# Performance work log

Measured on AMD Instinct MI355X. Metric: run time of the kernel, lower is better.

Reference implementation:

```python
import jax, jax.numpy as jnp
import numpy as np

N = 10                       # qubits
DIM = 2 ** N                 # statevector dim
B = 2048                     # batch
T = 8                        # timesteps
INV_SQRT = float(1.0 / np.sqrt(DIM))
H_GATE = jnp.asarray((1.0 / np.sqrt(2.0)) * np.array([[1, 1], [1, -1]], dtype=np.complex64))
T_GATE = jnp.asarray(np.array([[1, 0], [0, np.exp(1j * np.pi / 4)]], dtype=np.complex64))
# random CZ pairs in the candidate circuit are drawn once at circuit-build time (np.random > 0.7)
_rng = np.random.RandomState(0)
CAND_CZ = [(i, j) for i in range(N) for j in range(i + 1, N) if _rng.random() > 0.7]


def _ry(t):
    c, s = jnp.cos(t / 2), jnp.sin(t / 2)
    return jnp.stack([jnp.stack([c, -s], -1), jnp.stack([s, c], -1)], -2).astype(jnp.complex64)


def _rz(t):
    e = jnp.exp(-0.5j * t.astype(jnp.complex64))
    z = jnp.zeros_like(e)
    return jnp.stack([jnp.stack([e, z], -1), jnp.stack([z, jnp.conj(e)], -1)], -2)


def _rx(t):
    c = jnp.cos(t / 2).astype(jnp.complex64)
    s = (-1j * jnp.sin(t / 2).astype(jnp.complex64))
    return jnp.stack([jnp.stack([c, s], -1), jnp.stack([s, c], -1)], -2)


def _app1(st, q, U):
    # apply a 1-qubit gate on qubit q; U is [2,2] or batched [B,2,2]
    b = st.shape[0]
    s = st.reshape(b, 2 ** q, 2, DIM // 2 ** (q + 1))
    if U.ndim == 2:
        s = jnp.einsum('ij,bljr->blir', U, s)
    else:
        s = jnp.einsum('bij,bljr->blir', U, s)
    return s.reshape(b, DIM)


def _cz(st, q1, q2):  # q1 < q2
    b = st.shape[0]
    s = st.reshape(b, 2 ** q1, 2, 2 ** (q2 - q1 - 1), 2, DIM // 2 ** (q2 + 1))
    s = s.at[:, :, 1, :, 1, :].multiply(-1.0)
    return s.reshape(b, DIM)


def _cnot(st, qc, qt):  # qc < qt
    b = st.shape[0]
    s = st.reshape(b, 2 ** qc, 2, 2 ** (qt - qc - 1), 2, DIM // 2 ** (qt + 1))
    c0 = s[:, :, 0]                      # [b, A, M, 2, C]
    c1 = jnp.flip(s[:, :, 1], axis=3)    # flip target bit when control == 1
    return jnp.stack([c0, c1], axis=2).reshape(b, DIM)


def _uniform(b):
    # initialize_quantum_state: H on every qubit from |0...0> = uniform real state
    return jnp.full((b, DIM), INV_SQRT, dtype=jnp.complex64)


def _measure(st):
    # <Z>, <X>, <Y> per qubit (get_measurement_operators) -> [b, 3N]
    b = st.shape[0]
    feats = []
    for q in range(N):
        s = st.reshape(b, 2 ** q, 2, DIM // 2 ** (q + 1))
        a0, a1 = s[:, :, 0, :], s[:, :, 1, :]
        p0 = jnp.sum(jnp.abs(a0) ** 2, axis=(1, 2))
        p1 = jnp.sum(jnp.abs(a1) ** 2, axis=(1, 2))
        cr = jnp.sum(jnp.conj(a0) * a1, axis=(1, 2))
        feats += [p0 - p1, 2 * jnp.real(cr), 2 * jnp.imag(cr)]
    return jnp.stack(feats, -1)


def circ_forget(p):  # p [b, N]
    s = _uniform(p.shape[0])
    for q in range(N):
        s = _app1(s, q, _ry(p[:, q]))
    for q in range(0, N - 1, 2):
        s = _cz(s, q, q + 1)
    for q in range(N):
        s = _app1(s, q, T_GATE)
    return _measure(s)


def circ_input(p):  # p [b, 2N]
    s = _uniform(p.shape[0])
    for q in range(N):
        s = _app1(s, q, _ry(p[:, 2 * q]))
        s = _app1(s, q, _rz(p[:, 2 * q + 1]))
    for q in range(N - 1):
        s = _cnot(s, q, q + 1)
    return _measure(s)


def circ_output(p):  # p [b, N]
    s = _uniform(p.shape[0])
    for q in range(N):
        s = _app1(s, q, _rx(p[:, q]))
    for q in range(N - 1):
        s = _cnot(s, q, q + 1)
    return _measure(s)


def circ_candidate(p):  # p [b, 3N]
    s = _uniform(p.shape[0])
    for q in range(N):  # second H layer of the candidate gate
        s = _app1(s, q, H_GATE)
    for q in range(N):
        s = _app1(s, q, _rz(p[:, 3 * q]))
        s = _app1(s, q, _ry(p[:, 3 * q + 1]))
        s = _app1(s, q, _rz(p[:, 3 * q + 2]))
    for (i, j) in CAND_CZ:
        s = _cz(s, i, j)
    return _measure(s)


def circ_memory(p):  # p [b, N]
    s = _uniform(p.shape[0])
    for q in range(N):
        s = _app1(s, q, _ry(p[:, q]))
    for q in range(0, N - 1, 2):
        s = _cz(s, q, q + 1)
    return _measure(s)


def circ_temporal(t):  # t [b]
    s = _uniform(t.shape[0])
    nm = N // 2
    for i in range(min(nm, N - nm)):           # entangle memory<->hidden
        s = _cnot(s, i, nm + i)
    s = _app1(s, 0, H_GATE)                    # GHZ-style entanglement
    for i in range(1, N):
        s = _cnot(s, 0, i)
    for q in range(N):                         # time evolution
        s = _app1(s, q, _rz(0.1 * t))
        s = _app1(s, q, _rx(0.05 * t))
    for q in range(N - 1):
        s = _cnot(s, q, q + 1)
        s = _app1(s, q + 1, _rz(0.2 * t))
        s = _cnot(s, q, q + 1)
    return _measure(s)


def _forward(x, Wx, Wh, bias, R):
    Bsz = x.shape[0]

    def step(carry, x_t):
        h, c = carry
        p = x_t @ Wx + h @ Wh + bias            # [B, 8N+1] circuit angles
        pf, pi = p[:, :N], p[:, N:3 * N]
        po, pc = p[:, 3 * N:4 * N], p[:, 4 * N:7 * N]
        pm, pt = p[:, 7 * N:8 * N], p[:, 8 * N]
        f = jax.nn.sigmoid(circ_forget(pf) @ R[0])
        i_ = jax.nn.sigmoid(circ_input(pi) @ R[1])
        o = jax.nn.sigmoid(circ_output(po) @ R[2])
        g = jnp.tanh(circ_candidate(pc) @ R[3])
        mq = jax.nn.sigmoid(circ_memory(pm) @ R[4])
        tm = jnp.tanh(circ_temporal(pt) @ R[5])
        c_new = (f * c + i_ * g) * mq           # quantum memory update
        h_new = o * jnp.tanh(c_new) + 0.1 * tm  # temporal evolution contribution
        return (h_new, c_new), h_new

    h0 = jnp.zeros((Bsz, N), jnp.float32)
    c0 = jnp.zeros((Bsz, N), jnp.float32)
    _, hs = jax.lax.scan(step, (h0, c0), jnp.swapaxes(x, 0, 1))
    return jnp.swapaxes(hs, 0, 1)               # [B, T, N]


def setup_inputs() -> dict:
    key = jax.random.key(0)
    k1, k2, k3, k4 = jax.random.split(key, 4)
    x = jax.random.normal(k1, (B, T, N), dtype=jnp.float32)
    Wx = 0.3 * jax.random.normal(k2, (N, 8 * N + 1), dtype=jnp.float32)
    Wh = 0.3 * jax.random.normal(k3, (N, 8 * N + 1), dtype=jnp.float32)
    bias = jnp.zeros((8 * N + 1,), dtype=jnp.float32)
    R = 0.3 * jax.random.normal(k4, (6, 3 * N, N), dtype=jnp.float32)
    return {"x": x, "Wx": Wx, "Wh": Wh, "bias": bias, "R": R}


def reference(x, Wx, Wh, bias, R):
    return _forward(x, Wx, Wh, bias, R)
```

## Files before the change

### kernel.cpp

```cpp
#include <hip/hip_runtime.h>

#define NQ 10
#define NP 81
#define TT 8

__device__ __forceinline__ float sigm(float z) {
    z = fminf(fmaxf(z, -30.f), 30.f);
    return 1.f / (1.f + __expf(-z));
}
__device__ __forceinline__ float tanh_(float z) {
    z = fminf(fmaxf(z, -15.f), 15.f);
    float e = __expf(2.f * z);
    return (e - 1.f) / (e + 1.f);
}

__global__ __launch_bounds__(256) void qlstm_kernel(
    const float* __restrict__ x, const float* __restrict__ Wx,
    const float* __restrict__ Wh, const float* __restrict__ bias,
    const float* __restrict__ R, float* __restrict__ out) {

    __shared__ float x_s[8 * 8 * 12];
    __shared__ float h_s[8 * 12];
    __shared__ float c_s[8 * 10];
    __shared__ float p_s[8 * NP];
    __shared__ float ft_s[30 * 40];
    __shared__ float g_s[8 * 5 * 10];

    const int tid = threadIdx.x;
    const int bbase = blockIdx.x * 8;

    for (int i = tid; i < 640; i += 256) {
        int g = i / 80, r = i - g * 80;
        int t = r / 10, k = r - t * 10;
        x_s[g * 96 + t * 12 + k] = x[(size_t)bbase * 80 + i];
    }
    if (tid < 96) h_s[tid] = 0.f;
    if (tid < 80) c_s[tid] = 0.f;

    const int j1 = tid & 127;
    const int g0 = (tid >> 7) * 4;
    const bool p1act = (j1 < NP);
    float wx[NQ], wh[NQ], bj = 0.f;
    if (p1act) {
#pragma unroll
        for (int k = 0; k < NQ; ++k) { wx[k] = Wx[k * NP + j1]; wh[k] = Wh[k * NP + j1]; }
        bj = bias[j1];
    }

    const int gB1 = tid / 50, remB1 = tid - gB1 * 50;
    const int gt1 = remB1 / 10, k1 = remB1 - gt1 * 10;
    const int gR1 = gt1 + (gt1 >= 2 ? 1 : 0);
    float r1[30];
#pragma unroll
    for (int f = 0; f < 30; ++f) r1[f] = R[gR1 * 300 + f * 10 + k1];
    const bool hasj2 = (tid < 144);
    const int jb2 = tid + 256;
    const int gB2 = jb2 / 50, remB2 = jb2 - gB2 * 50;
    const int gt2 = remB2 / 10, k2 = remB2 - gt2 * 10;
    const int gR2 = gt2 + (gt2 >= 2 ? 1 : 0);
    float r2[30];
    if (hasj2) {
#pragma unroll
        for (int f = 0; f < 30; ++f) r2[f] = R[gR2 * 300 + f * 10 + k2];
    }

    const bool hasC = (tid < 80);
    const int gC = tid / 10, kC = tid - gC * 10;
    float o_val = 0.f;
    if (hasC) {
        float s = 0.f;
#pragma unroll
        for (int q = 0; q < NQ; ++q) s += R[600 + (3 * q + 1) * 10 + kC];
        o_val = sigm(s);
    }

    const int wv = tid >> 6, ln = tid & 63;
    __syncthreads();

    for (int t = 0; t < TT; ++t) {
        if (p1act) {
            float acc[4];
#pragma unroll
            for (int i = 0; i < 4; ++i) acc[i] = bj;
#pragma unroll
            for (int i = 0; i < 4; ++i) {
                const float* xr = &x_s[(g0 + i) * 96 + t * 12];
                const float* hr = &h_s[(g0 + i) * 12];
#pragma unroll
                for (int k = 0; k < NQ; ++k)
                    acc[i] = fmaf(xr[k], wx[k], fmaf(hr[k], wh[k], acc[i]));
            }
#pragma unroll
            for (int i = 0; i < 4; ++i) p_s[(g0 + i) * NP + j1] = acc[i];
        }
        __syncthreads();

        if (wv == 0 && ln < 8) {
            const int g = ln;
            const float* pp = &p_s[g * NP];
            float sa[NQ], ca[NQ], ftl[30];
#pragma unroll
            for (int q = 0; q < NQ; ++q) __sincosf(pp[q], &sa[q], &ca[q]);
            const float r2c = 0.70710678118654752f;
#pragma unroll
            for (int m = 0; m < 5; ++m) {
                int q = 2 * m, q1 = q + 1;
                ftl[3 * q] = -sa[q];
                float v = -r2c * ca[q] * sa[q1];
                ftl[3 * q + 1] = v; ftl[3 * q + 2] = v;
                ftl[3 * q1] = -sa[q1];
                float v2 = -r2c * ca[q1] * sa[q];
                ftl[3 * q1 + 1] = v2; ftl[3 * q1 + 2] = v2;
            }
#pragma unroll
            for (int f = 0; f < 30; ++f) ft_s[f * 40 + g * 5 + 0] = ftl[f];
        } else if (wv == 1 && ln < 8) {
            const int g = ln;
            const float* pp = &p_s[g * NP];
            float sa[NQ], ca[NQ], sb[NQ], cb[NQ], ftl[30];
#pragma unroll
            for (int q = 0; q < NQ; ++q) __sincosf(pp[10 + 2 * q], &sa[q], &ca[q]);
#pragma unroll
            for (int q = 0; q < NQ; ++q) __sincosf(pp[11 + 2 * q], &sb[q], &cb[q]);
            float xx[NQ], uu[NQ];
#pragma unroll
            for (int q = 0; q < NQ; ++q) { xx[q] = ca[q] * cb[q]; uu[q] = ca[q] * sb[q]; }
            float Zprev = 1.f;
#pragma unroll
            for (int q = 0; q < NQ; ++q) {
                float zq = Zprev * (-sa[q]);
                float xn = (q < 9) ? xx[q + 1] : 1.f;
                ftl[3 * q] = zq;
                ftl[3 * q + 1] = xx[q] * xn;
                ftl[3 * q + 2] = uu[q] * Zprev * xn;
                Zprev = zq;
            }
#pragma unroll
            for (int f = 0; f < 30; ++f) ft_s[f * 40 + g * 5 + 1] = ftl[f];
        } else if (wv == 2 && ln < 8) {
            const int g = ln;
            const float* pp = &p_s[g * NP];
            float sb[NQ], cb[NQ], sc[NQ], cc[NQ], ftl[30];
#pragma unroll
            for (int q = 0; q < NQ; ++q) __sincosf(pp[41 + 3 * q], &sb[q], &cb[q]);
#pragma unroll
            for (int q = 0; q < NQ; ++q) __sincosf(pp[42 + 3 * q], &sc[q], &cc[q]);
            float P[NQ];
            P[0] = cb[2] * cb[8] * cb[9];
            P[1] = cb[3] * cb[6];
            P[2] = cb[0] * cb[3] * cb[4] * cb[5] * cb[6] * cb[7] * cb[9];
            P[3] = cb[1] * cb[2] * cb[7];
            P[4] = cb[2] * cb[6];
            P[5] = cb[2] * cb[9];
            P[6] = cb[1] * cb[2] * cb[4];
            P[7] = cb[2] * cb[3];
            P[8] = cb[0];
            P[9] = cb[0] * cb[2] * cb[5];
#pragma unroll
            for (int q = 0; q < NQ; ++q) {
                ftl[3 * q] = cb[q];
                float m = sb[q] * P[q];
                ftl[3 * q + 1] = m * cc[q];
                ftl[3 * q + 2] = m * sc[q];
            }
#pragma unroll
            for (int f = 0; f < 30; ++f) ft_s[f * 40 + g * 5 + 2] = ftl[f];
        } else if (wv == 3 && ln < 16) {
            if (ln < 8) {
                const int g = ln;
                float tt = p_s[g * NP + 80];
                float s2, c2, s4, c4, s6, c6, s8, c8, ftl[30];
                __sincosf(0.050f * tt, &s2, &c2);
                __sincosf(0.100f * tt, &s4, &c4);
                __sincosf(0.150f * tt, &s6, &c6);
                __sincosf(0.200f * tt, &s8, &c8);
                (void)s4;
                float z0 = c2;
                float zs = 0.5f * (c2 - c6);
                float mre = 0.5f * c4;
                float mim = 0.25f * (s2 + s6);
                float E0re = c8, E0im = z0 * s8;
                float Esre = c8, Esim = zs * s8;
                float cr0re = 0.5f * s2 * Esim;
                float cr0im = -0.5f * s2 * Esre;
                float EEre = Esre * Esre - Esim * Esim, EEim = 2.f * Esre * Esim;
                float EOre = E0re * Esre - E0im * Esim, EOim = E0re * Esim + E0im * Esre;
                float cr1re = mre * EOre - mim * EOim, cr1im = mre * EOim + mim * EOre;
                float crmre = mre * EEre - mim * EEim, crmim = mre * EEim + mim * EEre;
                float cr9re = mre * Esre - mim * Esim, cr9im = mre * Esim + mim * Esre;
                ftl[0] = z0; ftl[1] = 2.f * cr0re; ftl[2] = 2.f * cr0im;
                ftl[3] = zs; ftl[4] = 2.f * cr1re; ftl[5] = 2.f * cr1im;
#pragma unroll
                for (int q = 2; q <= 8; ++q) {
                    ftl[3 * q] = zs; ftl[3 * q + 1] = 2.f * crmre; ftl[3 * q + 2] = 2.f * crmim;
                }
                ftl[27] = zs; ftl[28] = 2.f * cr9re; ftl[29] = 2.f * cr9im;
#pragma unroll
                for (int f = 0; f < 30; ++f) ft_s[f * 40 + g * 5 + 4] = ftl[f];
            } else {
                const int g = ln - 8;
                const float* pp = &p_s[g * NP];
                float sa[NQ], ca[NQ], ftl[30];
#pragma unroll
                for (int q = 0; q < NQ; ++q) __sincosf(pp[70 + q], &sa[q], &ca[q]);
#pragma unroll
                for (int m = 0; m < 5; ++m) {
                    int q = 2 * m, q1 = q + 1;
                    ftl[3 * q] = -sa[q];
                    ftl[3 * q + 1] = -ca[q] * sa[q1];
                    ftl[3 * q + 2] = 0.f;
                    ftl[3 * q1] = -sa[q1];
                    ftl[3 * q1 + 1] = -ca[q1] * sa[q];
                    ftl[3 * q1 + 2] = 0.f;
                }
#pragma unroll
                for (int f = 0; f < 30; ++f) ft_s[f * 40 + g * 5 + 3] = ftl[f];
            }
        }
        __syncthreads();

        {
            const int base1 = gB1 * 5 + gt1;
            float acc = 0.f;
#pragma unroll
            for (int f = 0; f < 30; ++f) acc = fmaf(ft_s[f * 40 + base1], r1[f], acc);
            g_s[tid] = acc;
            if (hasj2) {
                const int base2 = gB2 * 5 + gt2;
                float acc2 = 0.f;
#pragma unroll
                for (int f = 0; f < 30; ++f) acc2 = fmaf(ft_s[f * 40 + base2], r2[f], acc2);
                g_s[jb2] = acc2;
            }
        }
        __syncthreads();

        if (hasC) {
            float f = sigm(g_s[gC * 50 + 0 * 10 + kC]);
            float ii = sigm(g_s[gC * 50 + 1 * 10 + kC]);
            float gg = tanh_(g_s[gC * 50 + 2 * 10 + kC]);
            float mq = sigm(g_s[gC * 50 + 3 * 10 + kC]);
            float tm = tanh_(g_s[gC * 50 + 4 * 10 + kC]);
            float cn = (f * c_s[gC * 10 + kC] + ii * gg) * mq;
            float hn = o_val * tanh_(cn) + 0.1f * tm;
            c_s[gC * 10 + kC] = cn;
            h_s[gC * 12 + kC] = hn;
            out[(size_t)(bbase + gC) * 80 + t * 10 + kC] = hn;
        }
        __syncthreads();
    }
}

extern "C" void kernel_launch(void* const* d_in, const int* in_sizes, int n_in,
                              void* d_out, int out_size, void* d_ws, size_t ws_size,
                              hipStream_t stream) {
    const float* x = (const float*)d_in[0];
    const float* Wx = (const float*)d_in[1];
    const float* Wh = (const float*)d_in[2];
    const float* bias = (const float*)d_in[3];
    const float* R = (const float*)d_in[4];
    float* out = (float*)d_out;

    qlstm_kernel<<<dim3(256), dim3(256), 0, stream>>>(x, Wx, Wh, bias, R, out);
}
```

Measured before the change: 80.07 us.

## Map one batch element per wavefront and replace block barriers with wave-local sync

Restructures the recurrent kernel so each 64-lane wavefront owns one batch element, using wave barriers instead of block-wide __syncthreads. Input projections for all timesteps are precomputed before the loop. Per-lane sincos replaces the serial per-thread trig loops, and feature and gate stages are spread across lanes with float4 LDS reads. The grid doubles to 512 blocks for more parallelism. The cost is that more lanes sit idle in some stages, and correctness now depends on wave-synchronous LDS ordering.

```diff
diff --git a/kernel.cpp b/kernel.cpp
--- a/kernel.cpp
+++ b/kernel.cpp
@@ -3,6 +3,15 @@
 #define NQ 10
 #define NP 81
 #define TT 8
+
+#define PXO   0
+#define SOFF  648
+#define COFF  712
+#define FTO   776
+#define GOFF  956
+#define HOFF  1008
+#define XOFF  1020
+#define WWORDS 1100
 
 __device__ __forceinline__ float sigm(float z) {
     z = fminf(fmaxf(z, -30.f), 30.f);
@@ -19,235 +28,191 @@
     const float* __restrict__ Wh, const float* __restrict__ bias,
     const float* __restrict__ R, float* __restrict__ out) {
 
-    __shared__ float x_s[8 * 8 * 12];
-    __shared__ float h_s[8 * 12];
-    __shared__ float c_s[8 * 10];
-    __shared__ float p_s[8 * NP];
-    __shared__ float ft_s[30 * 40];
-    __shared__ float g_s[8 * 5 * 10];
-
+    __shared__ __align__(16) float lds_all[4 * WWORDS];
     const int tid = threadIdx.x;
-    const int bbase = blockIdx.x * 8;
-
-    for (int i = tid; i < 640; i += 256) {
-        int g = i / 80, r = i - g * 80;
-        int t = r / 10, k = r - t * 10;
-        x_s[g * 96 + t * 12 + k] = x[(size_t)bbase * 80 + i];
-    }
-    if (tid < 96) h_s[tid] = 0.f;
-    if (tid < 80) c_s[tid] = 0.f;
-
-    const int j1 = tid & 127;
-    const int g0 = (tid >> 7) * 4;
-    const bool p1act = (j1 < NP);
-    float wx[NQ], wh[NQ], bj = 0.f;
-    if (p1act) {
-#pragma unroll
-        for (int k = 0; k < NQ; ++k) { wx[k] = Wx[k * NP + j1]; wh[k] = Wh[k * NP + j1]; }
-        bj = bias[j1];
-    }
-
-    const int gB1 = tid / 50, remB1 = tid - gB1 * 50;
-    const int gt1 = remB1 / 10, k1 = remB1 - gt1 * 10;
-    const int gR1 = gt1 + (gt1 >= 2 ? 1 : 0);
-    float r1[30];
-#pragma unroll
-    for (int f = 0; f < 30; ++f) r1[f] = R[gR1 * 300 + f * 10 + k1];
-    const bool hasj2 = (tid < 144);
-    const int jb2 = tid + 256;
-    const int gB2 = jb2 / 50, remB2 = jb2 - gB2 * 50;
-    const int gt2 = remB2 / 10, k2 = remB2 - gt2 * 10;
-    const int gR2 = gt2 + (gt2 >= 2 ? 1 : 0);
-    float r2[30];
-    if (hasj2) {
-#pragma unroll
-        for (int f = 0; f < 30; ++f) r2[f] = R[gR2 * 300 + f * 10 + k2];
-    }
-
-    const bool hasC = (tid < 80);
-    const int gC = tid / 10, kC = tid - gC * 10;
+    const int wv = tid >> 6, ln = tid & 63;
+    float* lds = &lds_all[wv * WWORDS];
+    const int g = blockIdx.x * 4 + wv;
+
+    const float* xg = x + (size_t)g * 80;
+    lds[XOFF + ln] = xg[ln];
+    if (ln < 16) lds[XOFF + 64 + ln] = xg[64 + ln];
+
+    const int j1 = ln, j2 = 64 + ln;
+    const bool has2 = (ln < 17);
+    float wx1[NQ], wh1[NQ], wx2[NQ], wh2[NQ];
+    float b1 = bias[j1], b2 = 0.f;
+#pragma unroll
+    for (int k = 0; k < NQ; ++k) { wx1[k] = Wx[k * NP + j1]; wh1[k] = Wh[k * NP + j1]; }
+    if (has2) {
+        b2 = bias[j2];
+#pragma unroll
+        for (int k = 0; k < NQ; ++k) { wx2[k] = Wx[k * NP + j2]; wh2[k] = Wh[k * NP + j2]; }
+    } else {
+#pragma unroll
+        for (int k = 0; k < NQ; ++k) { wx2[k] = 0.f; wh2[k] = 0.f; }
+    }
+
+    __builtin_amdgcn_wave_barrier();
+#pragma unroll
+    for (int t = 0; t < TT; ++t) {
+        float a1 = b1, a2 = b2;
+#pragma unroll
+        for (int k = 0; k < NQ; ++k) {
+            float xv = lds[XOFF + t * 10 + k];
+            a1 = fmaf(xv, wx1[k], a1);
+            a2 = fmaf(xv, wx2[k], a2);
+        }
+        lds[PXO + t * NP + j1] = a1;
+        if (has2) lds[PXO + t * NP + j2] = a2;
+    }
+
+    int aidx; float amul = 1.f;
+    if (ln < 30) aidx = ln;
+    else if (ln < 50) { int u = ln - 30; aidx = 41 + 3 * (u >> 1) + (u & 1); }
+    else if (ln < 60) aidx = ln + 20;
+    else { aidx = 80; amul = 0.05f * (float)(ln - 59); }
+
+    const int c5 = ln / 10, q5 = ln - 10 * c5;
+    const unsigned cm = (q5 == 0) ? 0x304u : (q5 == 1) ? 0x048u : (q5 == 2) ? 0x2F9u :
+                        (q5 == 3) ? 0x086u : (q5 == 4) ? 0x044u : (q5 == 5) ? 0x204u :
+                        (q5 == 6) ? 0x016u : (q5 == 7) ? 0x00Cu : (q5 == 8) ? 0x001u : 0x025u;
+    unsigned pmsk = 0u; int pbase = SOFF + 10;
+    if (c5 == 1) pmsk = (1u << q5) - 1u;
+    else if (c5 == 2) { pmsk = cm; pbase = COFF + 30; }
+    int a0 = 60, a2i = 62, a4 = 61, a5 = 63;
+    if (c5 == 0)      { a0 = q5;          a2i = q5 ^ 1; }
+    else if (c5 == 1) { a0 = 10 + 2 * q5; a2i = 11 + 2 * q5;
+                        a4 = (q5 < 9) ? (12 + 2 * q5) : 61;
+                        a5 = (q5 < 9) ? (13 + 2 * q5) : 63; }
+    else if (c5 == 2) { a0 = 30 + 2 * q5; a2i = 31 + 2 * q5; }
+    else if (c5 == 3) { a0 = 50 + q5;     a2i = 50 + (q5 ^ 1); }
+
+    float rr[32];
+    if (ln < 50) {
+        const int gR = c5 + (c5 >= 2 ? 1 : 0);
+#pragma unroll
+        for (int f = 0; f < 30; ++f) rr[f] = R[gR * 300 + f * 10 + q5];
+    } else {
+#pragma unroll
+        for (int f = 0; f < 30; ++f) rr[f] = 0.f;
+    }
+    rr[30] = 0.f; rr[31] = 0.f;
+
     float o_val = 0.f;
-    if (hasC) {
+    if (ln < 10) {
         float s = 0.f;
 #pragma unroll
-        for (int q = 0; q < NQ; ++q) s += R[600 + (3 * q + 1) * 10 + kC];
+        for (int q = 0; q < NQ; ++q) s += R[600 + (3 * q + 1) * 10 + ln];
         o_val = sigm(s);
     }
 
-    const int wv = tid >> 6, ln = tid & 63;
-    __syncthreads();
-
+    if (ln < 30) lds[FTO + (ln / 6) * 36 + 30 + (ln % 6)] = 0.f;
+    if (ln < 12) lds[HOFF + ln] = 0.f;
+    float creg = 0.f;
+    __builtin_amdgcn_wave_barrier();
+
+    const float r2c = 0.70710678118654752f;
+    float* outg = out + (size_t)g * 80;
+
+#pragma unroll 1
     for (int t = 0; t < TT; ++t) {
-        if (p1act) {
-            float acc[4];
-#pragma unroll
-            for (int i = 0; i < 4; ++i) acc[i] = bj;
-#pragma unroll
-            for (int i = 0; i < 4; ++i) {
-                const float* xr = &x_s[(g0 + i) * 96 + t * 12];
-                const float* hr = &h_s[(g0 + i) * 12];
-#pragma unroll
-                for (int k = 0; k < NQ; ++k)
-                    acc[i] = fmaf(xr[k], wx[k], fmaf(hr[k], wh[k], acc[i]));
+        float p1v = lds[PXO + t * NP + j1];
+        float p2v = has2 ? lds[PXO + t * NP + j2] : 0.f;
+#pragma unroll
+        for (int k = 0; k < NQ; ++k) {
+            float hv = lds[HOFF + k];
+            p1v = fmaf(hv, wh1[k], p1v);
+            p2v = fmaf(hv, wh2[k], p2v);
+        }
+        __builtin_amdgcn_wave_barrier();
+
+        float va = __shfl(p1v, aidx & 63, 64);
+        float vb = __shfl(p2v, (aidx - 64) & 63, 64);
+        float ang = ((aidx < 64) ? va : vb) * amul;
+        float sv, cv;
+        __sincosf(ang, &sv, &cv);
+        lds[SOFF + ln] = sv;
+        lds[COFF + ln] = cv;
+        __builtin_amdgcn_wave_barrier();
+
+        if (ln < 50) {
+            float prod = 1.f;
+#pragma unroll
+            for (int i = 0; i < 10; ++i) {
+                float v = lds[pbase + 2 * i];
+                prod *= ((pmsk >> i) & 1u) ? v : 1.f;
             }
-#pragma unroll
-            for (int i = 0; i < 4; ++i) p_s[(g0 + i) * NP + j1] = acc[i];
-        }
-        __syncthreads();
-
-        if (wv == 0 && ln < 8) {
-            const int g = ln;
-            const float* pp = &p_s[g * NP];
-            float sa[NQ], ca[NQ], ftl[30];
-#pragma unroll
-            for (int q = 0; q < NQ; ++q) __sincosf(pp[q], &sa[q], &ca[q]);
-            const float r2c = 0.70710678118654752f;
-#pragma unroll
-            for (int m = 0; m < 5; ++m) {
-                int q = 2 * m, q1 = q + 1;
-                ftl[3 * q] = -sa[q];
-                float v = -r2c * ca[q] * sa[q1];
-                ftl[3 * q + 1] = v; ftl[3 * q + 2] = v;
-                ftl[3 * q1] = -sa[q1];
-                float v2 = -r2c * ca[q1] * sa[q];
-                ftl[3 * q1 + 1] = v2; ftl[3 * q1 + 2] = v2;
-            }
-#pragma unroll
-            for (int f = 0; f < 30; ++f) ft_s[f * 40 + g * 5 + 0] = ftl[f];
-        } else if (wv == 1 && ln < 8) {
-            const int g = ln;
-            const float* pp = &p_s[g * NP];
-            float sa[NQ], ca[NQ], sb[NQ], cb[NQ], ftl[30];
-#pragma unroll
-            for (int q = 0; q < NQ; ++q) __sincosf(pp[10 + 2 * q], &sa[q], &ca[q]);
-#pragma unroll
-            for (int q = 0; q < NQ; ++q) __sincosf(pp[11 + 2 * q], &sb[q], &cb[q]);
-            float xx[NQ], uu[NQ];
-#pragma unroll
-            for (int q = 0; q < NQ; ++q) { xx[q] = ca[q] * cb[q]; uu[q] = ca[q] * sb[q]; }
-            float Zprev = 1.f;
-#pragma unroll
-            for (int q = 0; q < NQ; ++q) {
-                float zq = Zprev * (-sa[q]);
-                float xn = (q < 9) ? xx[q + 1] : 1.f;
-                ftl[3 * q] = zq;
-                ftl[3 * q + 1] = xx[q] * xn;
-                ftl[3 * q + 2] = uu[q] * Zprev * xn;
-                Zprev = zq;
-            }
-#pragma unroll
-            for (int f = 0; f < 30; ++f) ft_s[f * 40 + g * 5 + 1] = ftl[f];
-        } else if (wv == 2 && ln < 8) {
-            const int g = ln;
-            const float* pp = &p_s[g * NP];
-            float sb[NQ], cb[NQ], sc[NQ], cc[NQ], ftl[30];
-#pragma unroll
-            for (int q = 0; q < NQ; ++q) __sincosf(pp[41 + 3 * q], &sb[q], &cb[q]);
-#pragma unroll
-            for (int q = 0; q < NQ; ++q) __sincosf(pp[42 + 3 * q], &sc[q], &cc[q]);
-            float P[NQ];
-            P[0] = cb[2] * cb[8] * cb[9];
-            P[1] = cb[3] * cb[6];
-            P[2] = cb[0] * cb[3] * cb[4] * cb[5] * cb[6] * cb[7] * cb[9];
-            P[3] = cb[1] * cb[2] * cb[7];
-            P[4] = cb[2] * cb[6];
-            P[5] = cb[2] * cb[9];
-            P[6] = cb[1] * cb[2] * cb[4];
-            P[7] = cb[2] * cb[3];
-            P[8] = cb[0];
-            P[9] = cb[0] * cb[2] * cb[5];
-#pragma unroll
-            for (int q = 0; q < NQ; ++q) {
-                ftl[3 * q] = cb[q];
-                float m = sb[q] * P[q];
-                ftl[3 * q + 1] = m * cc[q];
-                ftl[3 * q + 2] = m * sc[q];
-            }
-#pragma unroll
-            for (int f = 0; f < 30; ++f) ft_s[f * 40 + g * 5 + 2] = ftl[f];
-        } else if (wv == 3 && ln < 16) {
-            if (ln < 8) {
-                const int g = ln;
-                float tt = p_s[g * NP + 80];
-                float s2, c2, s4, c4, s6, c6, s8, c8, ftl[30];
-                __sincosf(0.050f * tt, &s2, &c2);
-                __sincosf(0.100f * tt, &s4, &c4);
-                __sincosf(0.150f * tt, &s6, &c6);
-                __sincosf(0.200f * tt, &s8, &c8);
-                (void)s4;
-                float z0 = c2;
-                float zs = 0.5f * (c2 - c6);
-                float mre = 0.5f * c4;
-                float mim = 0.25f * (s2 + s6);
-                float E0re = c8, E0im = z0 * s8;
-                float Esre = c8, Esim = zs * s8;
-                float cr0re = 0.5f * s2 * Esim;
-                float cr0im = -0.5f * s2 * Esre;
-                float EEre = Esre * Esre - Esim * Esim, EEim = 2.f * Esre * Esim;
-                float EOre = E0re * Esre - E0im * Esim, EOim = E0re * Esim + E0im * Esre;
+            float v0 = lds[SOFF + a0],  w0 = lds[COFF + a0];
+            float v2 = lds[SOFF + a2i], w2 = lds[COFF + a2i];
+            float w4 = lds[COFF + a4],  w5 = lds[COFF + a5];
+            float v6 = lds[SOFF + 63];
+            float f0, f1, f2;
+            if (c5 == 0) {
+                f0 = -v0; f1 = -r2c * w0 * v2; f2 = f1;
+            } else if (c5 == 1) {
+                float Z = (q5 & 1) ? -prod : prod;
+                float xn = (q5 < 9) ? w4 * w5 : 1.f;
+                f0 = -Z * v0;
+                f1 = (w0 * w2) * xn;
+                f2 = (w0 * v2) * (Z * xn);
+            } else if (c5 == 2) {
+                float m = v0 * prod;
+                f0 = w0; f1 = m * w2; f2 = m * v2;
+            } else if (c5 == 3) {
+                f0 = -v0; f1 = -w0 * v2; f2 = 0.f;
+            } else {
+                float s2 = v0, c2 = w0, s6 = v2, c6 = w2, c4v = w4, c8 = w5, s8 = v6;
+                float z0 = c2, zs = 0.5f * (c2 - c6);
+                float mre = 0.5f * c4v, mim = 0.25f * (s2 + s6);
+                float E0im = z0 * s8, Esim = zs * s8;
+                float cr0re = 0.5f * s2 * Esim, cr0im = -0.5f * s2 * c8;
+                float EEre = c8 * c8 - Esim * Esim, EEim = 2.f * c8 * Esim;
+                float EOre = c8 * c8 - E0im * Esim, EOim = c8 * Esim + E0im * c8;
                 float cr1re = mre * EOre - mim * EOim, cr1im = mre * EOim + mim * EOre;
                 float crmre = mre * EEre - mim * EEim, crmim = mre * EEim + mim * EEre;
-                float cr9re = mre * Esre - mim * Esim, cr9im = mre * Esim + mim * Esre;
-                ftl[0] = z0; ftl[1] = 2.f * cr0re; ftl[2] = 2.f * cr0im;
-                ftl[3] = zs; ftl[4] = 2.f * cr1re; ftl[5] = 2.f * cr1im;
-#pragma unroll
-                for (int q = 2; q <= 8; ++q) {
-                    ftl[3 * q] = zs; ftl[3 * q + 1] = 2.f * crmre; ftl[3 * q + 2] = 2.f * crmim;
-                }
-                ftl[27] = zs; ftl[28] = 2.f * cr9re; ftl[29] = 2.f * cr9im;
-#pragma unroll
-                for (int f = 0; f < 30; ++f) ft_s[f * 40 + g * 5 + 4] = ftl[f];
-            } else {
-                const int g = ln - 8;
-                const float* pp = &p_s[g * NP];
-                float sa[NQ], ca[NQ], ftl[30];
-#pragma unroll
-                for (int q = 0; q < NQ; ++q) __sincosf(pp[70 + q], &sa[q], &ca[q]);
-#pragma unroll
-                for (int m = 0; m < 5; ++m) {
-                    int q = 2 * m, q1 = q + 1;
-                    ftl[3 * q] = -sa[q];
-                    ftl[3 * q + 1] = -ca[q] * sa[q1];
-                    ftl[3 * q + 2] = 0.f;
-                    ftl[3 * q1] = -sa[q1];
-                    ftl[3 * q1 + 1] = -ca[q1] * sa[q];
-                    ftl[3 * q1 + 2] = 0.f;
-                }
-#pragma unroll
-                for (int f = 0; f < 30; ++f) ft_s[f * 40 + g * 5 + 3] = ftl[f];
+                float cr9re = mre * c8 - mim * Esim,  cr9im = mre * Esim + mim * c8;
+                f0 = (q5 == 0) ? z0 : zs;
+                float re = (q5 == 0) ? cr0re : (q5 == 1) ? cr1re : (q5 == 9) ? cr9re : crmre;
+                float im = (q5 == 0) ? cr0im : (q5 == 1) ? cr1im : (q5 == 9) ? cr9im : crmim;
+                f1 = 2.f * re; f2 = 2.f * im;
             }
-        }
-        __syncthreads();
-
-        {
-            const int base1 = gB1 * 5 + gt1;
-            float acc = 0.f;
-#pragma unroll
-            for (int f = 0; f < 30; ++f) acc = fmaf(ft_s[f * 40 + base1], r1[f], acc);
-            g_s[tid] = acc;
-            if (hasj2) {
-                const int base2 = gB2 * 5 + gt2;
-                float acc2 = 0.f;
-#pragma unroll
-                for (int f = 0; f < 30; ++f) acc2 = fmaf(ft_s[f * 40 + base2], r2[f], acc2);
-                g_s[jb2] = acc2;
+            const int fb = FTO + c5 * 36 + 3 * q5;
+            lds[fb] = f0; lds[fb + 1] = f1; lds[fb + 2] = f2;
+        }
+        __builtin_amdgcn_wave_barrier();
+
+        if (ln < 50) {
+            const float4* fp = (const float4*)&lds[FTO + c5 * 36];
+            float acc0 = 0.f, acc1 = 0.f;
+#pragma unroll
+            for (int f4 = 0; f4 < 8; f4 += 2) {
+                float4 u = fp[f4], w = fp[f4 + 1];
+                acc0 = fmaf(u.x, rr[4 * f4 + 0], acc0);
+                acc0 = fmaf(u.y, rr[4 * f4 + 1], acc0);
+                acc0 = fmaf(u.z, rr[4 * f4 + 2], acc0);
+                acc0 = fmaf(u.w, rr[4 * f4 + 3], acc0);
+                acc1 = fmaf(w.x, rr[4 * f4 + 4], acc1);
+                acc1 = fmaf(w.y, rr[4 * f4 + 5], acc1);
+                acc1 = fmaf(w.z, rr[4 * f4 + 6], acc1);
+                acc1 = fmaf(w.w, rr[4 * f4 + 7], acc1);
             }
-        }
-        __syncthreads();
-
-        if (hasC) {
-            float f = sigm(g_s[gC * 50 + 0 * 10 + kC]);
-            float ii = sigm(g_s[gC * 50 + 1 * 10 + kC]);
-            float gg = tanh_(g_s[gC * 50 + 2 * 10 + kC]);
-            float mq = sigm(g_s[gC * 50 + 3 * 10 + kC]);
-            float tm = tanh_(g_s[gC * 50 + 4 * 10 + kC]);
-            float cn = (f * c_s[gC * 10 + kC] + ii * gg) * mq;
-            float hn = o_val * tanh_(cn) + 0.1f * tm;
-            c_s[gC * 10 + kC] = cn;
-            h_s[gC * 12 + kC] = hn;
-            out[(size_t)(bbase + gC) * 80 + t * 10 + kC] = hn;
-        }
-        __syncthreads();
+            lds[GOFF + ln] = acc0 + acc1;
+        }
+        __builtin_amdgcn_wave_barrier();
+
+        if (ln < 10) {
+            float fz = sigm(lds[GOFF + ln]);
+            float iz = sigm(lds[GOFF + 10 + ln]);
+            float gz = tanh_(lds[GOFF + 20 + ln]);
+            float mz = sigm(lds[GOFF + 30 + ln]);
+            float tz = tanh_(lds[GOFF + 40 + ln]);
+            creg = (fz * creg + iz * gz) * mz;
+            float hn = o_val * tanh_(creg) + 0.1f * tz;
+            lds[HOFF + ln] = hn;
+            outg[t * 10 + ln] = hn;
+        }
+        __builtin_amdgcn_wave_barrier();
     }
 }
 
@@ -261,5 +226,5 @@
     const float* R = (const float*)d_in[4];
     float* out = (float*)d_out;
 
-    qlstm_kernel<<<dim3(256), dim3(256), 0, stream>>>(x, Wx, Wh, bias, R, out);
-}
+    qlstm_kernel<<<dim3(512), dim3(256), 0, stream>>>(x, Wx, Wh, bias, R, out);
+}
```

Measured after the change: 76.99 us. 3.8% less time.
